# Kernel optimization log

Hardware: AMD Instinct MI355X
Metric: run time of the kernel (lower is better)

The kernel has to match this reference:

```python
import jax, jax.numpy as jnp
import numpy as np

NUM_HEADS = 6
LOCAL_KS = 3


def setup_inputs() -> dict:
    key = jax.random.key(0)
    k1, k2, k3, k4 = jax.random.split(key, 4)
    B, N, C = 8, 1024, 384
    x = jax.random.normal(k1, (B, N, C), dtype=jnp.float32)
    qkv_w = jax.random.normal(k2, (3 * C, C), dtype=jnp.float32) * (C ** -0.5)
    proj_w = jax.random.normal(k3, (C, C), dtype=jnp.float32) * (C ** -0.5)
    proj_b = jax.random.normal(k4, (C,), dtype=jnp.float32) * 0.01
    return {"x": x, "qkv_w": qkv_w, "proj_w": proj_w, "proj_b": proj_b}


def reference(x, qkv_w, proj_w, proj_b):
    B, N, C = x.shape
    H = NUM_HEADS
    hd = C // H
    scale = hd ** -0.5
    half = LOCAL_KS // 2

    # qkv projection: [B,N,3C] -> q,k,v each [B,H,N,hd]
    qkv = (x @ qkv_w.T).reshape(B, N, 3, H, hd).transpose(2, 0, 3, 1, 4)
    q, k, v = qkv[0], qkv[1], qkv[2]

    # dense scores with banded local mask (clamped window == |i-j| <= half)
    attn = jnp.einsum('bhqd,bhkd->bhqk', q, k) * scale
    idx = jnp.arange(N)
    mask = jnp.abs(idx[:, None] - idx[None, :]) > half  # True -> masked out
    attn = jnp.where(mask, -jnp.inf, attn)
    p = jax.nn.softmax(attn, axis=-1)

    # AV then merge heads: [B,N,C]
    out = jnp.einsum('bhqk,bhkd->bqhd', p, v).reshape(B, N, C)
    return out @ proj_w.T + proj_b
```

## Files before the change

### kernel.cpp

```cpp
#include <hip/hip_runtime.h>
#include <hip/hip_bf16.h>
#include <math.h>

#define C_DIM 384
#define NHEADS 6
#define HD 64
#define BATCH 8
#define NSEQ 1024
#define M_ROWS (BATCH * NSEQ)

typedef __attribute__((ext_vector_type(4))) float f32x4;
typedef __attribute__((ext_vector_type(8))) short s16x8;

__device__ __forceinline__ float bf2f(short u) {
  return __uint_as_float(((unsigned)(unsigned short)u) << 16);
}
__device__ __forceinline__ short f2bf(float f) {
  __hip_bfloat16 h = __float2bfloat16(f);
  return *reinterpret_cast<short*>(&h);
}

__device__ __forceinline__ void gload_lds16(const void* g, void* l) {
  __builtin_amdgcn_global_load_lds(
      (const __attribute__((address_space(1))) unsigned int*)g,
      (__attribute__((address_space(3))) unsigned int*)l, 16, 0, 0);
}

template<int N> __device__ __forceinline__ void wait_vm() {
  if constexpr (N == 0) asm volatile("s_waitcnt vmcnt(0)" ::: "memory");
  else if constexpr (N == 3) asm volatile("s_waitcnt vmcnt(3)" ::: "memory");
  else if constexpr (N == 4) asm volatile("s_waitcnt vmcnt(4)" ::: "memory");
}

__global__ __launch_bounds__(256) void cast_all(
    const float* __restrict__ x, const float* __restrict__ qw,
    const float* __restrict__ pw,
    ushort4* __restrict__ xo, ushort4* __restrict__ qo, ushort4* __restrict__ po) {
  const int NX = M_ROWS * C_DIM / 4;
  const int NQ = 3 * C_DIM * C_DIM / 4;
  const int NP = C_DIM * C_DIM / 4;
  const int total = NX + NQ + NP;
  int idx = blockIdx.x * blockDim.x + threadIdx.x;
  int stride = gridDim.x * blockDim.x;
  for (int i = idx; i < total; i += stride) {
    const float4* s;
    ushort4* d;
    int off;
    if (i < NX) { s = (const float4*)x; d = xo; off = i; }
    else if (i < NX + NQ) { s = (const float4*)qw; d = qo; off = i - NX; }
    else { s = (const float4*)pw; d = po; off = i - NX - NQ; }
    float4 v = s[off];
    ushort4 o;
    o.x = (unsigned short)f2bf(v.x);
    o.y = (unsigned short)f2bf(v.y);
    o.z = (unsigned short)f2bf(v.z);
    o.w = (unsigned short)f2bf(v.w);
    d[off] = o;
  }
}

template<int BN, bool OUT_BF16>
__global__ __launch_bounds__(256) void gemm_db(
    const __hip_bfloat16* __restrict__ A,
    const __hip_bfloat16* __restrict__ W,
    const float* __restrict__ bias,
    void* __restrict__ outp,
    int M, int N, int K) {
  constexpr int NF = BN / 32;
  constexpr int BPT = (BN * 32 / 8) / 256;
  constexpr int LPS = 2 + BPT;
  __shared__ __align__(16) __hip_bfloat16 As[2][128 * 32];
  __shared__ __align__(16) __hip_bfloat16 Bs[2][BN * 32];

  const int tid = threadIdx.x;
  const int nwg = gridDim.x * gridDim.y;
  const int bid0 = blockIdx.y * gridDim.x + blockIdx.x;
  const int cpx = nwg >> 3;
  const int wg = (bid0 & 7) * cpx + (bid0 >> 3);
  const int bx = wg % gridDim.x;
  const int by = wg / gridDim.x;

  const int lane = tid & 63;
  const int wave = tid >> 6;
  const int wr = (wave >> 1) * 64;
  const int wc = (wave & 1) * (BN / 2);
  const int rowBase = by * 128;
  const int colBase = bx * BN;

  const int l16 = lane & 15;
  const int lk8 = (lane >> 4) * 8;
  const int lr4 = (lane >> 4) * 4;

  f32x4 acc[4][NF] = {};

  const int nkt = K >> 5;

  auto stage = [&](int buf, int kt) {
    const int k0 = kt * 32;
#pragma unroll
    for (int i = 0; i < 2; ++i) {
      int c = tid + i * 256;
      int r = c >> 2, cc = (c & 3) * 8;
      gload_lds16(A + (size_t)(rowBase + r) * K + k0 + cc, &As[buf][c * 8]);
    }
#pragma unroll
    for (int i = 0; i < BPT; ++i) {
      int c = tid + i * 256;
      int r = c >> 2, cc = (c & 3) * 8;
      gload_lds16(W + (size_t)(colBase + r) * K + k0 + cc, &Bs[buf][c * 8]);
    }
  };

  stage(0, 0);
  for (int kt = 0; kt < nkt; ++kt) {
    const int cur = kt & 1;
    if (kt + 1 < nkt) {
      stage(cur ^ 1, kt + 1);
      wait_vm<LPS>();
    } else {
      wait_vm<0>();
    }
    __builtin_amdgcn_sched_barrier(0);
    __builtin_amdgcn_s_barrier();
    __builtin_amdgcn_sched_barrier(0);

    s16x8 af[4], bfr[NF];
#pragma unroll
    for (int m = 0; m < 4; ++m)
      af[m] = *(const s16x8*)(&As[cur][(wr + m * 16 + l16) * 32 + lk8]);
#pragma unroll
    for (int n = 0; n < NF; ++n)
      bfr[n] = *(const s16x8*)(&Bs[cur][(wc + n * 16 + l16) * 32 + lk8]);
#pragma unroll
    for (int m = 0; m < 4; ++m)
#pragma unroll
      for (int n = 0; n < NF; ++n)
        acc[m][n] = __builtin_amdgcn_mfma_f32_16x16x32_bf16(
            af[m], bfr[n], acc[m][n], 0, 0, 0);

    __builtin_amdgcn_sched_barrier(0);
    __builtin_amdgcn_s_barrier();
    __builtin_amdgcn_sched_barrier(0);
  }

#pragma unroll
  for (int m = 0; m < 4; ++m) {
    int rb = rowBase + wr + m * 16 + lr4;
#pragma unroll
    for (int n = 0; n < NF; ++n) {
      int cb = colBase + wc + n * 16 + l16;
#pragma unroll
      for (int j = 0; j < 4; ++j) {
        float v = acc[m][n][j];
        if (OUT_BF16) {
          ((__hip_bfloat16*)outp)[(size_t)(rb + j) * N + cb] = __float2bfloat16(v);
        } else {
          ((float*)outp)[(size_t)(rb + j) * N + cb] = v + bias[cb];
        }
      }
    }
  }
}

__global__ __launch_bounds__(256) void local_attn_v3(
    const __hip_bfloat16* __restrict__ qkv, __hip_bfloat16* __restrict__ attn_out) {
  __shared__ __align__(16) ushort lds[24832];
  const int QOFF = 0;
  const int KOFF = 8192;
  const int VOFF = 8192 + 8320;

  const int tid = threadIdx.x;
  const int mb = blockIdx.x & 63;
  const int h  = blockIdx.x >> 6;
  const int rb = mb * 128;
  const int b  = rb >> 10;
  const int n0 = rb & 1023;
  const int RS = 3 * C_DIM;

#pragma unroll
  for (int i = 0; i < 4; ++i) {
    int s = i * 256 + tid;
    int r = s >> 3;
    int jg = (s & 7) ^ (r & 7);
    gload_lds16(qkv + (size_t)(rb + r) * RS + h * HD + jg * 8,
                lds + QOFF + s * 8);
  }
#pragma unroll
  for (int i = 0; i < 5; ++i) {
    int s = i * 256 + tid;
    if (s < 1040) {
      int r = s >> 3;
      int jg = (s & 7) ^ (r & 7);
      int nl = n0 + r - 1;
      nl = nl < 0 ? 0 : (nl > 1023 ? 1023 : nl);
      size_t row = (size_t)(b << 10) + nl;
      gload_lds16(qkv + row * RS + C_DIM + h * HD + jg * 8, lds + KOFF + s * 8);
      gload_lds16(qkv + row * RS + 2 * C_DIM + h * HD + jg * 8, lds + VOFF + s * 8);
    }
  }
  __syncthreads();

  const int r = tid >> 1;
  const int half = tid & 1;
  const int jbase = half * 4;
  const int n = n0 + r;

  float qf[32];
#pragma unroll
  for (int c = 0; c < 4; ++c) {
    int slot = r * 8 + ((jbase + c) ^ (r & 7));
    s16x8 v = *(const s16x8*)(lds + QOFF + slot * 8);
#pragma unroll
    for (int e = 0; e < 8; ++e) qf[c * 8 + e] = bf2f(v[e]);
  }

  float s3[3];
#pragma unroll
  for (int jj = 0; jj < 3; ++jj) {
    int krow = r + jj;
    float acc = 0.f;
#pragma unroll
    for (int c = 0; c < 4; ++c) {
      int slot = krow * 8 + ((jbase + c) ^ (krow & 7));
      s16x8 v = *(const s16x8*)(lds + KOFF + slot * 8);
#pragma unroll
      for (int e = 0; e < 8; ++e) acc += qf[c * 8 + e] * bf2f(v[e]);
    }
    acc += __shfl_xor(acc, 1);
    s3[jj] = ((unsigned)(n + jj - 1) < (unsigned)NSEQ) ? acc * 0.125f : -1e30f;
  }

  float mx = fmaxf(s3[0], fmaxf(s3[1], s3[2]));
  float p0 = __expf(s3[0] - mx);
  float p1 = __expf(s3[1] - mx);
  float p2 = __expf(s3[2] - mx);
  float inv = 1.f / (p0 + p1 + p2);
  float p[3] = {p0 * inv, p1 * inv, p2 * inv};

  float of[32] = {};
#pragma unroll
  for (int jj = 0; jj < 3; ++jj) {
    int krow = r + jj;
    float pw = p[jj];
#pragma unroll
    for (int c = 0; c < 4; ++c) {
      int slot = krow * 8 + ((jbase + c) ^ (krow & 7));
      s16x8 v = *(const s16x8*)(lds + VOFF + slot * 8);
#pragma unroll
      for (int e = 0; e < 8; ++e) of[c * 8 + e] += pw * bf2f(v[e]);
    }
  }

#pragma unroll
  for (int c = 0; c < 4; ++c) {
    s16x8 o;
#pragma unroll
    for (int e = 0; e < 8; ++e) o[e] = f2bf(of[c * 8 + e]);
    *(s16x8*)(attn_out + (size_t)(rb + r) * C_DIM + h * HD + jbase * 8 + c * 8) = o;
  }
}

extern "C" void kernel_launch(void* const* d_in, const int* in_sizes, int n_in,
                              void* d_out, int out_size, void* d_ws, size_t ws_size,
                              hipStream_t stream) {
  const float* x      = (const float*)d_in[0];
  const float* qkv_w  = (const float*)d_in[1];
  const float* proj_w = (const float*)d_in[2];
  const float* proj_b = (const float*)d_in[3];
  float* out = (float*)d_out;

  __hip_bfloat16* x_bf     = (__hip_bfloat16*)d_ws;
  __hip_bfloat16* qkvw_bf  = x_bf + (size_t)M_ROWS * C_DIM;
  __hip_bfloat16* projw_bf = qkvw_bf + (size_t)3 * C_DIM * C_DIM;
  __hip_bfloat16* qkv_bf   = projw_bf + (size_t)C_DIM * C_DIM;
  __hip_bfloat16* attn_bf  = qkv_bf + (size_t)M_ROWS * 3 * C_DIM;

  cast_all<<<1024, 256, 0, stream>>>(
      x, qkv_w, proj_w, (ushort4*)x_bf, (ushort4*)qkvw_bf, (ushort4*)projw_bf);

  gemm_db<128, true><<<dim3((3 * C_DIM) / 128, M_ROWS / 128), 256, 0, stream>>>(
      x_bf, qkvw_bf, nullptr, qkv_bf, M_ROWS, 3 * C_DIM, C_DIM);

  local_attn_v3<<<64 * NHEADS, 256, 0, stream>>>(qkv_bf, attn_bf);

  gemm_db<64, false><<<dim3(C_DIM / 64, M_ROWS / 128), 256, 0, stream>>>(
      attn_bf, projw_bf, proj_b, out, M_ROWS, C_DIM, C_DIM);
}
```

Measured before the change: 43.98 us.

## Fuse fp32-to-bf16 casts into GEMM staging and drop the separate cast kernel

Removes the standalone cast kernel. Both GEMMs now load fp32 inputs and weights into registers, convert them to bf16, and write them to LDS. This avoids a full extra read and write pass over x and the weights plus one kernel launch. The QKV GEMM moves to 512 threads with a register-prefetch pipeline. The cost is that each GEMM block re-reads and re-converts the fp32 weight tiles, and register staging replaces async global-to-LDS loads, which may reduce overlap.

```diff
diff --git a/kernel.cpp b/kernel.cpp
--- a/kernel.cpp
+++ b/kernel.cpp
@@ -19,6 +19,12 @@
   __hip_bfloat16 h = __float2bfloat16(f);
   return *reinterpret_cast<short*>(&h);
 }
+__device__ __forceinline__ s16x8 cvt8(float4 a, float4 b) {
+  s16x8 r;
+  r[0] = f2bf(a.x); r[1] = f2bf(a.y); r[2] = f2bf(a.z); r[3] = f2bf(a.w);
+  r[4] = f2bf(b.x); r[5] = f2bf(b.y); r[6] = f2bf(b.z); r[7] = f2bf(b.w);
+  return r;
+}
 
 __device__ __forceinline__ void gload_lds16(const void* g, void* l) {
   __builtin_amdgcn_global_load_lds(
@@ -26,51 +32,23 @@
       (__attribute__((address_space(3))) unsigned int*)l, 16, 0, 0);
 }
 
-template<int N> __device__ __forceinline__ void wait_vm() {
-  if constexpr (N == 0) asm volatile("s_waitcnt vmcnt(0)" ::: "memory");
-  else if constexpr (N == 3) asm volatile("s_waitcnt vmcnt(3)" ::: "memory");
-  else if constexpr (N == 4) asm volatile("s_waitcnt vmcnt(4)" ::: "memory");
-}
-
-__global__ __launch_bounds__(256) void cast_all(
-    const float* __restrict__ x, const float* __restrict__ qw,
-    const float* __restrict__ pw,
-    ushort4* __restrict__ xo, ushort4* __restrict__ qo, ushort4* __restrict__ po) {
-  const int NX = M_ROWS * C_DIM / 4;
-  const int NQ = 3 * C_DIM * C_DIM / 4;
-  const int NP = C_DIM * C_DIM / 4;
-  const int total = NX + NQ + NP;
-  int idx = blockIdx.x * blockDim.x + threadIdx.x;
-  int stride = gridDim.x * blockDim.x;
-  for (int i = idx; i < total; i += stride) {
-    const float4* s;
-    ushort4* d;
-    int off;
-    if (i < NX) { s = (const float4*)x; d = xo; off = i; }
-    else if (i < NX + NQ) { s = (const float4*)qw; d = qo; off = i - NX; }
-    else { s = (const float4*)pw; d = po; off = i - NX - NQ; }
-    float4 v = s[off];
-    ushort4 o;
-    o.x = (unsigned short)f2bf(v.x);
-    o.y = (unsigned short)f2bf(v.y);
-    o.z = (unsigned short)f2bf(v.z);
-    o.w = (unsigned short)f2bf(v.w);
-    d[off] = o;
-  }
-}
-
-template<int BN, bool OUT_BF16>
-__global__ __launch_bounds__(256) void gemm_db(
-    const __hip_bfloat16* __restrict__ A,
-    const __hip_bfloat16* __restrict__ W,
-    const float* __restrict__ bias,
-    void* __restrict__ outp,
-    int M, int N, int K) {
-  constexpr int NF = BN / 32;
-  constexpr int BPT = (BN * 32 / 8) / 256;
-  constexpr int LPS = 2 + BPT;
+__device__ __forceinline__ void wait_vm0() {
+  asm volatile("s_waitcnt vmcnt(0)" ::: "memory");
+}
+__device__ __forceinline__ void lgkm0() {
+  asm volatile("s_waitcnt lgkmcnt(0)" ::: "memory");
+}
+__device__ __forceinline__ void bar() {
+  __builtin_amdgcn_sched_barrier(0);
+  __builtin_amdgcn_s_barrier();
+  __builtin_amdgcn_sched_barrier(0);
+}
+
+__global__ __launch_bounds__(512) void gemm1_rs(
+    const float* __restrict__ A, const float* __restrict__ W,
+    __hip_bfloat16* __restrict__ outp, int M, int N, int K) {
   __shared__ __align__(16) __hip_bfloat16 As[2][128 * 32];
-  __shared__ __align__(16) __hip_bfloat16 Bs[2][BN * 32];
+  __shared__ __align__(16) __hip_bfloat16 Bs[2][128 * 32];
 
   const int tid = threadIdx.x;
   const int nwg = gridDim.x * gridDim.y;
@@ -82,82 +60,156 @@
 
   const int lane = tid & 63;
   const int wave = tid >> 6;
-  const int wr = (wave >> 1) * 64;
-  const int wc = (wave & 1) * (BN / 2);
+  const int wr = (wave >> 2) * 64;
+  const int wc = (wave & 3) * 32;
   const int rowBase = by * 128;
-  const int colBase = bx * BN;
-
+  const int colBase = bx * 128;
   const int l16 = lane & 15;
   const int lk8 = (lane >> 4) * 8;
   const int lr4 = (lane >> 4) * 4;
 
-  f32x4 acc[4][NF] = {};
-
+  const int sr = tid >> 2;
+  const int sc = (tid & 3) * 8;
+  const float* aSrc = A + (size_t)(rowBase + sr) * K + sc;
+  const float* bSrc = W + (size_t)(colBase + sr) * K + sc;
+
+  f32x4 acc[4][2] = {};
+  float4 aL[2], bL[2];
+
+  auto loadRegs = [&](int kt) {
+    const float4* ap = (const float4*)(aSrc + kt * 32);
+    aL[0] = ap[0]; aL[1] = ap[1];
+    const float4* bp = (const float4*)(bSrc + kt * 32);
+    bL[0] = bp[0]; bL[1] = bp[1];
+  };
+
+  loadRegs(0);
   const int nkt = K >> 5;
-
-  auto stage = [&](int buf, int kt) {
-    const int k0 = kt * 32;
+  for (int kt = 0; kt < nkt; ++kt) {
+    const int cur = kt & 1;
+    wait_vm0();
+    __builtin_amdgcn_sched_barrier(0);
+    *(s16x8*)&As[cur][sr * 32 + sc] = cvt8(aL[0], aL[1]);
+    *(s16x8*)&Bs[cur][sr * 32 + sc] = cvt8(bL[0], bL[1]);
+    if (kt + 1 < nkt) loadRegs(kt + 1);
+    lgkm0();
+    bar();
+
+    s16x8 af[4], bfr[2];
+#pragma unroll
+    for (int m = 0; m < 4; ++m)
+      af[m] = *(const s16x8*)(&As[cur][(wr + m * 16 + l16) * 32 + lk8]);
+#pragma unroll
+    for (int n = 0; n < 2; ++n)
+      bfr[n] = *(const s16x8*)(&Bs[cur][(wc + n * 16 + l16) * 32 + lk8]);
+#pragma unroll
+    for (int m = 0; m < 4; ++m)
+#pragma unroll
+      for (int n = 0; n < 2; ++n)
+        acc[m][n] = __builtin_amdgcn_mfma_f32_16x16x32_bf16(
+            af[m], bfr[n], acc[m][n], 0, 0, 0);
+    bar();
+  }
+
+#pragma unroll
+  for (int m = 0; m < 4; ++m) {
+    int rb = rowBase + wr + m * 16 + lr4;
+#pragma unroll
+    for (int n = 0; n < 2; ++n) {
+      int cb = colBase + wc + n * 16 + l16;
+#pragma unroll
+      for (int j = 0; j < 4; ++j)
+        outp[(size_t)(rb + j) * N + cb] = __float2bfloat16(acc[m][n][j]);
+    }
+  }
+}
+
+__global__ __launch_bounds__(256) void gemm2_mix(
+    const __hip_bfloat16* __restrict__ A, const float* __restrict__ W,
+    const float* __restrict__ bias, float* __restrict__ outp,
+    int M, int N, int K) {
+  __shared__ __align__(16) __hip_bfloat16 As[2][128 * 32];
+  __shared__ __align__(16) __hip_bfloat16 Bs[2][64 * 32];
+
+  const int tid = threadIdx.x;
+  const int nwg = gridDim.x * gridDim.y;
+  const int bid0 = blockIdx.y * gridDim.x + blockIdx.x;
+  const int cpx = nwg >> 3;
+  const int wg = (bid0 & 7) * cpx + (bid0 >> 3);
+  const int bx = wg % gridDim.x;
+  const int by = wg / gridDim.x;
+
+  const int lane = tid & 63;
+  const int wave = tid >> 6;
+  const int wr = (wave >> 1) * 64;
+  const int wc = (wave & 1) * 32;
+  const int rowBase = by * 128;
+  const int colBase = bx * 64;
+  const int l16 = lane & 15;
+  const int lk8 = (lane >> 4) * 8;
+  const int lr4 = (lane >> 4) * 4;
+
+  const int sr = tid >> 2;
+  const int sc = (tid & 3) * 8;
+  const float* bSrc = W + (size_t)(colBase + sr) * K + sc;
+
+  f32x4 acc[4][2] = {};
+  float4 bL[2];
+
+  auto stageA = [&](int kt, int buf) {
 #pragma unroll
     for (int i = 0; i < 2; ++i) {
       int c = tid + i * 256;
       int r = c >> 2, cc = (c & 3) * 8;
-      gload_lds16(A + (size_t)(rowBase + r) * K + k0 + cc, &As[buf][c * 8]);
-    }
-#pragma unroll
-    for (int i = 0; i < BPT; ++i) {
-      int c = tid + i * 256;
-      int r = c >> 2, cc = (c & 3) * 8;
-      gload_lds16(W + (size_t)(colBase + r) * K + k0 + cc, &Bs[buf][c * 8]);
+      gload_lds16(A + (size_t)(rowBase + r) * K + kt * 32 + cc, &As[buf][c * 8]);
     }
   };
-
-  stage(0, 0);
+  auto loadB = [&](int kt) {
+    const float4* bp = (const float4*)(bSrc + kt * 32);
+    bL[0] = bp[0]; bL[1] = bp[1];
+  };
+
+  stageA(0, 0);
+  loadB(0);
+  const int nkt = K >> 5;
   for (int kt = 0; kt < nkt; ++kt) {
     const int cur = kt & 1;
+    wait_vm0();
+    __builtin_amdgcn_sched_barrier(0);
+    *(s16x8*)&Bs[cur][sr * 32 + sc] = cvt8(bL[0], bL[1]);
     if (kt + 1 < nkt) {
-      stage(cur ^ 1, kt + 1);
-      wait_vm<LPS>();
-    } else {
-      wait_vm<0>();
-    }
-    __builtin_amdgcn_sched_barrier(0);
-    __builtin_amdgcn_s_barrier();
-    __builtin_amdgcn_sched_barrier(0);
-
-    s16x8 af[4], bfr[NF];
+      stageA(kt + 1, cur ^ 1);
+      loadB(kt + 1);
+    }
+    lgkm0();
+    bar();
+
+    s16x8 af[4], bfr[2];
 #pragma unroll
     for (int m = 0; m < 4; ++m)
       af[m] = *(const s16x8*)(&As[cur][(wr + m * 16 + l16) * 32 + lk8]);
 #pragma unroll
-    for (int n = 0; n < NF; ++n)
+    for (int n = 0; n < 2; ++n)
       bfr[n] = *(const s16x8*)(&Bs[cur][(wc + n * 16 + l16) * 32 + lk8]);
 #pragma unroll
     for (int m = 0; m < 4; ++m)
 #pragma unroll
-      for (int n = 0; n < NF; ++n)
+      for (int n = 0; n < 2; ++n)
         acc[m][n] = __builtin_amdgcn_mfma_f32_16x16x32_bf16(
             af[m], bfr[n], acc[m][n], 0, 0, 0);
-
-    __builtin_amdgcn_sched_barrier(0);
-    __builtin_amdgcn_s_barrier();
-    __builtin_amdgcn_sched_barrier(0);
+    bar();
   }
 
 #pragma unroll
   for (int m = 0; m < 4; ++m) {
     int rb = rowBase + wr + m * 16 + lr4;
 #pragma unroll
-    for (int n = 0; n < NF; ++n) {
+    for (int n = 0; n < 2; ++n) {
       int cb = colBase + wc + n * 16 + l16;
-#pragma unroll
-      for (int j = 0; j < 4; ++j) {
-        float v = acc[m][n][j];
-        if (OUT_BF16) {
-          ((__hip_bfloat16*)outp)[(size_t)(rb + j) * N + cb] = __float2bfloat16(v);
-        } else {
-          ((float*)outp)[(size_t)(rb + j) * N + cb] = v + bias[cb];
-        }
-      }
+      float bv = bias[cb];
+#pragma unroll
+      for (int j = 0; j < 4; ++j)
+        outp[(size_t)(rb + j) * N + cb] = acc[m][n][j] + bv;
     }
   }
 }
@@ -269,20 +321,14 @@
   const float* proj_b = (const float*)d_in[3];
   float* out = (float*)d_out;
 
-  __hip_bfloat16* x_bf     = (__hip_bfloat16*)d_ws;
-  __hip_bfloat16* qkvw_bf  = x_bf + (size_t)M_ROWS * C_DIM;
-  __hip_bfloat16* projw_bf = qkvw_bf + (size_t)3 * C_DIM * C_DIM;
-  __hip_bfloat16* qkv_bf   = projw_bf + (size_t)C_DIM * C_DIM;
-  __hip_bfloat16* attn_bf  = qkv_bf + (size_t)M_ROWS * 3 * C_DIM;
-
-  cast_all<<<1024, 256, 0, stream>>>(
-      x, qkv_w, proj_w, (ushort4*)x_bf, (ushort4*)qkvw_bf, (ushort4*)projw_bf);
-
-  gemm_db<128, true><<<dim3((3 * C_DIM) / 128, M_ROWS / 128), 256, 0, stream>>>(
-      x_bf, qkvw_bf, nullptr, qkv_bf, M_ROWS, 3 * C_DIM, C_DIM);
+  __hip_bfloat16* qkv_bf  = (__hip_bfloat16*)d_ws;
+  __hip_bfloat16* attn_bf = qkv_bf + (size_t)M_ROWS * 3 * C_DIM;
+
+  gemm1_rs<<<dim3(9, 64), 512, 0, stream>>>(
+      x, qkv_w, qkv_bf, M_ROWS, 3 * C_DIM, C_DIM);
 
   local_attn_v3<<<64 * NHEADS, 256, 0, stream>>>(qkv_bf, attn_bf);
 
-  gemm_db<64, false><<<dim3(C_DIM / 64, M_ROWS / 128), 256, 0, stream>>>(
-      attn_bf, projw_bf, proj_b, out, M_ROWS, C_DIM, C_DIM);
-}
+  gemm2_mix<<<dim3(6, 64), 256, 0, stream>>>(
+      attn_bf, proj_w, proj_b, out, M_ROWS, C_DIM, C_DIM);
+}
```

After: 42.85 us, median of 2. 2.6% less time.
